# Optimization experiments

Measured on AMD Instinct MI355X. Metric: run time of the kernel, lower is better.

## Reference

```python
import jax, jax.numpy as jnp
import numpy as np

B, N, D = 8, 2048, 768
LN_EPS = 1e-5


def setup_inputs() -> dict:
    key = jax.random.key(0)
    ks = jax.random.split(key, 5)
    scale = 1.0 / np.sqrt(D)
    features = jax.random.normal(ks[0], (B, N, D), dtype=jnp.float32)
    mask = jax.random.randint(ks[1], (B, N), 0, 2) == 1  # True = masked (padding)
    Wq = jax.random.normal(ks[2], (D, D), dtype=jnp.float32) * scale
    Wk = jax.random.normal(ks[3], (D, D), dtype=jnp.float32) * scale
    Wv = jax.random.normal(ks[4], (D, D), dtype=jnp.float32) * scale
    ln_gamma = jnp.ones((D,), dtype=jnp.float32)
    ln_beta = jnp.zeros((D,), dtype=jnp.float32)
    return {"features": features, "mask": mask, "Wq": Wq, "Wk": Wk, "Wv": Wv,
            "ln_gamma": ln_gamma, "ln_beta": ln_beta}


def reference(features, mask, Wq, Wk, Wv, ln_gamma, ln_beta):
    # LayerNorm over last dim
    mu = jnp.mean(features, axis=-1, keepdims=True)
    var = jnp.mean(jnp.square(features - mu), axis=-1, keepdims=True)
    x = (features - mu) * jax.lax.rsqrt(var + LN_EPS) * ln_gamma + ln_beta
    # torch Linear: y = x @ W.T
    Q = jnp.einsum('bnd,ed->bne', x, Wq)
    K = jnp.einsum('bnd,ed->bne', x, Wk)
    V = jnp.einsum('bnd,ed->bne', x, Wv)
    scale = x.shape[-1] ** -0.5
    scores = jnp.einsum('bnd,bmd->bnm', Q, K) * scale  # [B,N,N]
    scores = jnp.where(mask[:, None, :], -jnp.inf, scores)
    probs = jax.nn.softmax(scores, axis=-1)
    ctx = jnp.einsum('bnm,bmd->bnd', probs, V)
    return ctx
```

## Files before the change

kernel.cpp:

```cpp
#include <hip/hip_runtime.h>
#include <hip/hip_bf16.h>
#include <cstdint>

typedef __attribute__((ext_vector_type(8))) __bf16 bf16v8;
typedef __attribute__((ext_vector_type(4))) float f32x4;
typedef __attribute__((ext_vector_type(4))) unsigned short ushort4v;
typedef __attribute__((ext_vector_type(8))) unsigned short ushort8v;

#define BB 8
#define NN 2048
#define DD 768

__device__ __forceinline__ float b2f(unsigned short u) {
  union { unsigned int i; float f; } c; c.i = ((unsigned int)u) << 16; return c.f;
}
__device__ __forceinline__ unsigned short f2b(float f) {
  union { float f; unsigned int i; } c; c.f = f;
  unsigned int u = c.i;
  return (unsigned short)((u + 0x7fffu + ((u >> 16) & 1u)) >> 16);
}

__global__ __launch_bounds__(256) void ln_kernel(const float* __restrict__ x,
                                                 const float* __restrict__ gamma,
                                                 const float* __restrict__ beta,
                                                 unsigned short* __restrict__ xb) {
  int row = blockIdx.x;
  const float* xr = x + (size_t)row * DD;
  int t = threadIdx.x;
  float a0 = xr[t], a1 = xr[t + 256], a2 = xr[t + 512];
  float s = a0 + a1 + a2;
  float q = a0 * a0 + a1 * a1 + a2 * a2;
  for (int o = 32; o > 0; o >>= 1) { s += __shfl_xor(s, o); q += __shfl_xor(q, o); }
  __shared__ float red[2][4];
  int w = t >> 6, lane = t & 63;
  if (lane == 0) { red[0][w] = s; red[1][w] = q; }
  __syncthreads();
  s = red[0][0] + red[0][1] + red[0][2] + red[0][3];
  q = red[1][0] + red[1][1] + red[1][2] + red[1][3];
  float mean = s * (1.0f / DD);
  float var = q * (1.0f / DD) - mean * mean;
  float inv = rsqrtf(var + 1e-5f);
  unsigned short* o0 = xb + (size_t)row * DD;
  o0[t]       = f2b((a0 - mean) * inv * gamma[t]       + beta[t]);
  o0[t + 256] = f2b((a1 - mean) * inv * gamma[t + 256] + beta[t + 256]);
  o0[t + 512] = f2b((a2 - mean) * inv * gamma[t + 512] + beta[t + 512]);
}

__global__ __launch_bounds__(256) void wconvert(const float* __restrict__ Wq,
                                                const float* __restrict__ Wk,
                                                const float* __restrict__ Wv,
                                                unsigned short* __restrict__ Wcat) {
  int i = blockIdx.x * 256 + threadIdx.x;
  const int dd = DD * DD;
  if (i >= 3 * dd) return;
  float v;
  if (i < dd)           v = Wq[i] * 0.03608439182435161f;
  else if (i < 2 * dd)  v = Wk[i - dd];
  else                  v = Wv[i - 2 * dd];
  Wcat[i] = f2b(v);
}

__global__ __launch_bounds__(256) void mask_scan(const int* __restrict__ mask,
                                                 int* __restrict__ kidx,
                                                 int* __restrict__ ncnt) {
  int b = blockIdx.x;
  const int* mr = mask + b * NN;
  int t = threadIdx.x;
#pragma unroll
  for (int j = 0; j < 8; ++j) kidx[b * NN + t * 8 + j] = 0;
  int v[8]; int s = 0;
#pragma unroll
  for (int j = 0; j < 8; ++j) { v[j] = (mr[t * 8 + j] == 0) ? 1 : 0; s += v[j]; }
  int lane = t & 63, w = t >> 6;
  int x = s;
  for (int o = 1; o < 64; o <<= 1) { int y = __shfl_up(x, o); if (lane >= o) x += y; }
  __shared__ int wsum[4];
  if (lane == 63) wsum[w] = x;
  __syncthreads();
  int base = 0;
#pragma unroll
  for (int i = 0; i < 4; ++i) if (i < w) base += wsum[i];
  int run = base + x - s;
#pragma unroll
  for (int j = 0; j < 8; ++j) { if (v[j]) kidx[b * NN + run] = t * 8 + j; run += v[j]; }
  if (t == 255) ncnt[b] = base + x;
}

__global__ __launch_bounds__(256) void vtc_gather(const unsigned short* __restrict__ Vt,
                                                  const int* __restrict__ kidx,
                                                  const int* __restrict__ ncnt,
                                                  unsigned short* __restrict__ Vtc) {
  int be = blockIdx.x;
  int b = be / DD;
  int nc = ncnt[b];
  int r128 = (nc + 127) & ~127;
  const unsigned short* src = Vt + (size_t)be * NN;
  unsigned short* dst = Vtc + (size_t)be * NN;
  const int* kx = kidx + b * NN;
  for (int c = threadIdx.x; c < r128; c += 256)
    dst[c] = (c < nc) ? src[kx[c]] : (unsigned short)0;
}

__device__ __forceinline__ void gload_lds16(const void* g, void* l) {
  __builtin_amdgcn_global_load_lds(
      (const __attribute__((address_space(1))) void*)g,
      (__attribute__((address_space(3))) void*)(unsigned)(uintptr_t)l,
      16, 0, 0);
}

#define RDA(i0, ks, B)                                                                   \
  _Pragma("unroll")                                                                      \
  for (int i_ = 0; i_ < 4; ++i_)                                                         \
    aq[i_] = *(const bf16v8*)&smem[(B) + (ks) * 8192 + arow0 + ((i0) + i_) * 512 + kg8];
#define RDB(ks, B)                                                                       \
  _Pragma("unroll")                                                                      \
  for (int j_ = 0; j_ < NJ; ++j_)                                                        \
    bq[j_] = *(const bf16v8*)&smem[(B) + 16384 + (ks) * 8192 + brow0 + j_ * 512 + kg8];
#define MFQ(i0)                                                                          \
  _Pragma("unroll")                                                                      \
  for (int i_ = 0; i_ < 4; ++i_) {                                                       \
    _Pragma("unroll")                                                                    \
    for (int j_ = 0; j_ < NJ; ++j_)                                                      \
      acc[(i0) + i_][j_] = __builtin_amdgcn_mfma_f32_16x16x32_bf16(                      \
          aq[i_], bq[j_], acc[(i0) + i_][j_], 0, 0, 0);                                  \
  }
#define BARF asm volatile("s_barrier" ::: "memory")
#define VMC6 asm volatile("s_waitcnt vmcnt(6)" ::: "memory")
#define VMC0 asm volatile("s_waitcnt vmcnt(0)" ::: "memory")
#define P1   __builtin_amdgcn_s_setprio(1)
#define P0   __builtin_amdgcn_s_setprio(0)

#define TILEK(KT, CURB, NXTB)                                                            \
  do {                                                                                   \
    RDA(0, 0, CURB); RDB(0, CURB);                                                       \
    if ((KT) + 1 < NT) stgA((KT) + 1, 1, (NXTB));                                        \
    BARF; P1; MFQ(0); P0; BARF;                                                          \
    RDA(4, 0, CURB);                                                                     \
    if ((KT) + 1 < NT) stgB((KT) + 1, 1, (NXTB));                                        \
    BARF; P1; MFQ(4); P0;                                                                \
    VMC6; BARF;                                                                          \
    RDA(0, 1, CURB); RDB(1, CURB);                                                       \
    if ((KT) + 2 < NT) stgA((KT) + 2, 0, (CURB));                                        \
    BARF; P1; MFQ(0); P0; BARF;                                                          \
    RDA(4, 1, CURB);                                                                     \
    if ((KT) + 2 < NT) stgB((KT) + 2, 0, (CURB));                                        \
    BARF; P1; MFQ(4); P0;                                                                \
    if ((KT) < NT - 2) { VMC6; } else { VMC0; }                                          \
    BARF;                                                                                \
  } while (0)

template <int MODE, int NJ>
__global__ __launch_bounds__(512, 2) void gemm256(
    const unsigned short* __restrict__ A, const unsigned short* __restrict__ Bm,
    unsigned short* __restrict__ Cq, unsigned short* __restrict__ Ck,
    unsigned short* __restrict__ Cv, float* __restrict__ Cf,
    int K, int lda, int ldb,
    long aStride, long bStride, long cStride,
    const int* __restrict__ ncnt) {
  extern __shared__ unsigned short smem[];
  const int BN = NJ * 64;

  const int t = threadIdx.x;
  int bx = blockIdx.x, by = blockIdx.y, bz = blockIdx.z;
  {
    const int gx = gridDim.x, gy = gridDim.y;
    const int nwg = gx * gy * (int)gridDim.z;
    int id = bx + gx * (by + gy * bz);
    int sw = (id & 7) * (nwg >> 3) + (id >> 3);
    bx = sw % gx; int r2 = sw / gx;
    by = r2 % gy; bz = r2 / gy;
  }
  const int n0 = bx * BN, m0 = by * 256;
  const int NT = (MODE == 2) ? (((ncnt[bz] + 127) >> 7) << 1) : (K >> 6);

  const unsigned short* Ab = A + (size_t)bz * aStride;
  const unsigned short* Bb = Bm + (size_t)bz * bStride;

  const int lane = t & 63;
  const int w = t >> 6;
  const int wm = w >> 2, wn = w & 3;
  const int frow = lane & 15;
  const int kg8 = (lane >> 4) * 8;
  const int arow0 = (wm * 128 + frow) * 32;
  const int brow0 = (wn * (NJ * 16) + frow) * 32;

  const int srow = t >> 2;
  const int scol8 = (t & 3) * 8;
  const unsigned short* Asrc = Ab + (size_t)(m0 + srow) * lda + scol8;
  const unsigned short* Bsrc = Bb + (size_t)(n0 + srow) * ldb + scol8;
  const int sdst = w * 512;

  auto stgA = [&](int kt, int ks, int bufb) {
    const unsigned short* s = Asrc + kt * 64 + ks * 32;
    gload_lds16(s, &smem[bufb + ks * 8192 + sdst]);
    gload_lds16(s + (size_t)128 * lda, &smem[bufb + ks * 8192 + 4096 + sdst]);
  };
  auto stgB = [&](int kt, int ks, int bufb) {
    const unsigned short* s = Bsrc + kt * 64 + ks * 32;
    gload_lds16(s, &smem[bufb + 16384 + ks * 8192 + sdst]);
    gload_lds16(s + (size_t)128 * ldb, &smem[bufb + 16384 + ks * 8192 + 4096 + sdst]);
  };

  f32x4 acc[8][NJ] = {};
  bf16v8 aq[4], bq[NJ];

  stgA(0, 0, 0);     stgB(0, 0, 0);
  stgA(0, 1, 0);     stgB(0, 1, 0);
  stgA(1, 0, 32768); stgB(1, 0, 32768);
  asm volatile("s_waitcnt vmcnt(8)" ::: "memory");
  BARF;

  for (int ktp = 0; ktp < NT; ktp += 2) {
    TILEK(ktp, 0, 32768);
    TILEK(ktp + 1, 32768, 0);
  }

  const int r0 = (lane >> 4) * 4;
  const int c0 = lane & 15;
  const int mrowB = m0 + wm * 128 + r0;
  const int ncolB = n0 + wn * (NJ * 16) + c0;

  if (MODE == 0) {
    if (n0 < 1536) {
      unsigned short* dst = (n0 < 768) ? Cq : Ck;
      const int cb = (n0 < 768) ? 0 : 768;
#pragma unroll
      for (int i = 0; i < 8; ++i)
#pragma unroll
        for (int j = 0; j < NJ; ++j)
#pragma unroll
          for (int r = 0; r < 4; ++r)
            dst[(size_t)(mrowB + i * 16 + r) * DD + (ncolB + j * 16 - cb)] = f2b(acc[i][j][r]);
    } else {
#pragma unroll
      for (int i = 0; i < 8; ++i) {
        int row = mrowB + i * 16;
        int bb = row >> 11, nn = row & 2047;
#pragma unroll
        for (int j = 0; j < NJ; ++j) {
          int e = ncolB + j * 16 - 1536;
          ushort4v pk;
#pragma unroll
          for (int r = 0; r < 4; ++r) pk[r] = f2b(acc[i][j][r]);
          *(ushort4v*)&Cv[((size_t)(bb * DD + e)) * NN + nn] = pk;
        }
      }
    }
  } else {
    float* dst = Cf + (size_t)bz * cStride;
#pragma unroll
    for (int i = 0; i < 8; ++i)
#pragma unroll
      for (int j = 0; j < NJ; ++j)
#pragma unroll
        for (int r = 0; r < 4; ++r)
          dst[(size_t)(mrowB + i * 16 + r) * DD + (ncolB + j * 16)] = acc[i][j][r];
  }
}

template <int NJ, int NTT>
__global__ __launch_bounds__(512, 2) void gemm1P(
    const unsigned short* __restrict__ Qa, const unsigned short* __restrict__ Kn,
    unsigned short* __restrict__ So, const int* __restrict__ kidx,
    const int* __restrict__ ncnt, int lda, int ldb) {
  extern __shared__ unsigned short smem[];
  constexpr int NT = NTT;

  const int t = threadIdx.x;
  const int lane = t & 63;
  const int w = t >> 6;
  const int wm = w >> 2, wn = w & 3;
  const int frow = lane & 15;
  const int kg8 = (lane >> 4) * 8;
  const int arow0 = (wm * 128 + frow) * 32;
  const int brow0 = (wn * (NJ * 16) + frow) * 32;
  const int srow = t >> 2;
  const int scol8 = (t & 3) * 8;
  const int sdst = w * 512;
  const int r0 = (lane >> 4) * 4;
  const int c0 = lane & 15;

  int nbv[8];
#pragma unroll
  for (int b_ = 0; b_ < 8; ++b_) nbv[b_] = (ncnt[b_] + 255) >> 8;

  f32x4 acc[8][NJ];
  bf16v8 aq[4], bq[NJ];

#pragma unroll 1
  for (int it = 0; it < 2; ++it) {
    int rem = (int)blockIdx.x + it * 256;
    int b = 0;
#pragma unroll 1
    for (; b < 8; ++b) { int c = nbv[b] * 8; if (rem < c) break; rem -= c; }
    if (b >= 8) break;
    const int ni = rem >> 3, mi = rem & 7;
    const int m0 = mi * 256, n0 = ni * 256;

    const unsigned short* Asrc = Qa + ((size_t)b * NN + m0 + srow) * lda + scol8;
    const int kv0 = kidx[b * NN + n0 + srow];
    const int kv1 = kidx[b * NN + n0 + 128 + srow];
    const unsigned short* Bsrc0 = Kn + ((size_t)b * NN + kv0) * ldb + scol8;
    const unsigned short* Bsrc1 = Kn + ((size_t)b * NN + kv1) * ldb + scol8;

    auto stgA = [&](int kt, int ks, int bufb) {
      const unsigned short* s = Asrc + kt * 64 + ks * 32;
      gload_lds16(s, &smem[bufb + ks * 8192 + sdst]);
      gload_lds16(s + (size_t)128 * lda, &smem[bufb + ks * 8192 + 4096 + sdst]);
    };
    auto stgB = [&](int kt, int ks, int bufb) {
      gload_lds16(Bsrc0 + kt * 64 + ks * 32, &smem[bufb + 16384 + ks * 8192 + sdst]);
      gload_lds16(Bsrc1 + kt * 64 + ks * 32, &smem[bufb + 16384 + ks * 8192 + 4096 + sdst]);
    };

#pragma unroll
    for (int i = 0; i < 8; ++i)
#pragma unroll
      for (int j = 0; j < NJ; ++j) acc[i][j] = f32x4{0.f, 0.f, 0.f, 0.f};

    stgA(0, 0, 0);     stgB(0, 0, 0);
    stgA(0, 1, 0);     stgB(0, 1, 0);
    stgA(1, 0, 32768); stgB(1, 0, 32768);
    asm volatile("s_waitcnt vmcnt(8)" ::: "memory");
    BARF;

    for (int ktp = 0; ktp < NT; ktp += 2) {
      TILEK(ktp, 0, 32768);
      TILEK(ktp + 1, 32768, 0);
    }

    unsigned short* dst = So + (size_t)b * NN * NN;
    const int mrowB = m0 + wm * 128 + r0;
    const int ncolB = n0 + wn * (NJ * 16) + c0;
#pragma unroll
    for (int i = 0; i < 8; ++i)
#pragma unroll
      for (int j = 0; j < NJ; ++j)
#pragma unroll
        for (int r = 0; r < 4; ++r)
          dst[(size_t)(mrowB + i * 16 + r) * NN + (ncolB + j * 16)] = f2b(acc[i][j][r]);
  }
}

__global__ __launch_bounds__(256) void softmax_c(unsigned short* __restrict__ S,
                                                 const int* __restrict__ ncnt) {
  int row = blockIdx.x;
  int bb = row >> 11;
  const int nc = ncnt[bb];
  const int p128 = (nc + 127) & ~127;
  unsigned short* sr = S + (size_t)row * NN;
  int t = threadIdx.x;
  const int cbase = t * 8;

  float v[8];
  const bool anyload = cbase < nc;
  ushort8v pk;
  if (anyload) pk = *(const ushort8v*)&sr[cbase];
  float mx = -1e30f;
#pragma unroll
  for (int j = 0; j < 8; ++j) {
    v[j] = anyload ? b2f(pk[j]) : 0.f;
    if (cbase + j < nc) mx = fmaxf(mx, v[j]);
  }
  for (int o = 32; o > 0; o >>= 1) mx = fmaxf(mx, __shfl_xor(mx, o));
  __shared__ float redm[4], reds[4];
  int w = t >> 6, lane = t & 63;
  if (lane == 0) redm[w] = mx;
  __syncthreads();
  mx = fmaxf(fmaxf(redm[0], redm[1]), fmaxf(redm[2], redm[3]));

  float e[8];
  float sum = 0.f;
#pragma unroll
  for (int j = 0; j < 8; ++j) {
    e[j] = (cbase + j < nc) ? __expf(v[j] - mx) : 0.f;
    sum += e[j];
  }
  for (int o = 32; o > 0; o >>= 1) sum += __shfl_xor(sum, o);
  if (lane == 0) reds[w] = sum;
  __syncthreads();
  sum = reds[0] + reds[1] + reds[2] + reds[3];
  float inv = 1.0f / sum;

  if (cbase < p128) {
    ushort8v op;
#pragma unroll
    for (int j = 0; j < 8; ++j) op[j] = f2b(e[j] * inv);
    *(ushort8v*)&sr[cbase] = op;
  }
}

extern "C" void kernel_launch(void* const* d_in, const int* in_sizes, int n_in,
                              void* d_out, int out_size, void* d_ws, size_t ws_size,
                              hipStream_t stream) {
  const float* features = (const float*)d_in[0];
  const int* mask       = (const int*)d_in[1];
  const float* Wq       = (const float*)d_in[2];
  const float* Wk       = (const float*)d_in[3];
  const float* Wv       = (const float*)d_in[4];
  const float* gamma    = (const float*)d_in[5];
  const float* beta     = (const float*)d_in[6];
  float* out = (float*)d_out;

  char* ws = (char*)d_ws;
  size_t off = 0;
  auto alloc = [&](size_t bytes) {
    char* p = ws + off;
    off += (bytes + 255) & ~(size_t)255;
    return p;
  };
  unsigned short* Wcat = (unsigned short*)alloc((size_t)(2304 + 64) * DD * 2);
  unsigned short* Qb   = (unsigned short*)alloc((size_t)BB * NN * DD * 2);
  unsigned short* Kb   = (unsigned short*)alloc((size_t)BB * NN * DD * 2);
  unsigned short* Vt   = (unsigned short*)alloc(((size_t)BB * DD + 64) * NN * 2);
  int* kidx = (int*)alloc((size_t)BB * NN * 4);
  int* ncnt = (int*)alloc(64 * 4);
  char* last = alloc((size_t)BB * NN * NN * 2);
  unsigned short* Sb = (unsigned short*)last;
  unsigned short* Xb = (unsigned short*)last;
  unsigned short* Vtc = Qb;

  (void)hipFuncSetAttribute(reinterpret_cast<const void*>(&gemm256<0, 3>),
                            hipFuncAttributeMaxDynamicSharedMemorySize, 131072);
  (void)hipFuncSetAttribute(reinterpret_cast<const void*>(&gemm1P<4, 12>),
                            hipFuncAttributeMaxDynamicSharedMemorySize, 131072);
  (void)hipFuncSetAttribute(reinterpret_cast<const void*>(&gemm256<2, 3>),
                            hipFuncAttributeMaxDynamicSharedMemorySize, 131072);

  ln_kernel<<<BB * NN, 256, 0, stream>>>(features, gamma, beta, Xb);
  wconvert<<<(3 * DD * DD + 255) / 256, 256, 0, stream>>>(Wq, Wk, Wv, Wcat);
  mask_scan<<<BB, 256, 0, stream>>>(mask, kidx, ncnt);

  gemm256<0, 3><<<dim3(2304 / 192, (BB * NN) / 256, 1), 512, 131072, stream>>>(
      Xb, Wcat, Qb, Kb, Vt, nullptr, DD, DD, DD, 0, 0, 0, ncnt);

  gemm1P<4, 12><<<256, 512, 131072, stream>>>(Qb, Kb, Sb, kidx, ncnt, DD, DD);

  vtc_gather<<<BB * DD, 256, 0, stream>>>(Vt, kidx, ncnt, Vtc);

  softmax_c<<<BB * NN, 256, 0, stream>>>(Sb, ncnt);

  gemm256<2, 3><<<dim3(DD / 192, NN / 256, BB), 512, 131072, stream>>>(
      Sb, Vtc, nullptr, nullptr, nullptr, out, NN, NN, NN,
      (long)NN * NN, (long)DD * NN, (long)NN * DD, ncnt);
}
```

Measured before the change: 225.1 us.

## Compute K and V projections only for unmasked keys via compacted inputs

Unmasked rows of the normalized input are gathered into a compacted buffer first. A dedicated K/V projection GEMM then runs only over those rows and writes compacted K and transposed V directly, while the Q projection stays a separate full GEMM. This drops the index-gathered B loads in the score GEMM and the separate V gather kernel, and skips projecting masked keys (about half of them). It adds a new gather kernel and per-batch offset bookkeeping, and splits the one fused QKV launch into two.

```diff
diff --git a/kernel.cpp b/kernel.cpp
--- a/kernel.cpp
+++ b/kernel.cpp
@@ -86,19 +86,31 @@
   if (t == 255) ncnt[b] = base + x;
 }
 
-__global__ __launch_bounds__(256) void vtc_gather(const unsigned short* __restrict__ Vt,
-                                                  const int* __restrict__ kidx,
-                                                  const int* __restrict__ ncnt,
-                                                  unsigned short* __restrict__ Vtc) {
-  int be = blockIdx.x;
-  int b = be / DD;
-  int nc = ncnt[b];
-  int r128 = (nc + 127) & ~127;
-  const unsigned short* src = Vt + (size_t)be * NN;
-  unsigned short* dst = Vtc + (size_t)be * NN;
-  const int* kx = kidx + b * NN;
-  for (int c = threadIdx.x; c < r128; c += 256)
-    dst[c] = (c < nc) ? src[kx[c]] : (unsigned short)0;
+__global__ __launch_bounds__(256) void xc_gather(const unsigned short* __restrict__ Xb,
+                                                 const int* __restrict__ kidx,
+                                                 const int* __restrict__ ncnt,
+                                                 unsigned short* __restrict__ Xc) {
+  const int b = blockIdx.y;
+  const int nc = ncnt[b];
+  const int r256 = (nc + 255) & ~255;
+  const int row0 = blockIdx.x * 32;
+  if (row0 >= r256) return;
+  int off = 0;
+#pragma unroll
+  for (int i = 0; i < 8; ++i) if (i < b) off += (ncnt[i] + 255) & ~255;
+  const int t = threadIdx.x;
+  for (int r = 0; r < 32; ++r) {
+    const int rl = row0 + r;
+    unsigned short* dst = Xc + (size_t)(off + rl) * DD;
+    if (t < 96) {
+      if (rl < nc) {
+        const unsigned short* src = Xb + ((size_t)b * NN + kidx[b * NN + rl]) * DD;
+        *(ushort8v*)&dst[t * 8] = *(const ushort8v*)&src[t * 8];
+      } else {
+        *(ushort8v*)&dst[t * 8] = ushort8v{0, 0, 0, 0, 0, 0, 0, 0};
+      }
+    }
+  }
 }
 
 __device__ __forceinline__ void gload_lds16(const void* g, void* l) {
@@ -152,8 +164,7 @@
 template <int MODE, int NJ>
 __global__ __launch_bounds__(512, 2) void gemm256(
     const unsigned short* __restrict__ A, const unsigned short* __restrict__ Bm,
-    unsigned short* __restrict__ Cq, unsigned short* __restrict__ Ck,
-    unsigned short* __restrict__ Cv, float* __restrict__ Cf,
+    unsigned short* __restrict__ Cq, float* __restrict__ Cf,
     int K, int lda, int ldb,
     long aStride, long bStride, long cStride,
     const int* __restrict__ ncnt) {
@@ -220,49 +231,120 @@
   const int mrowB = m0 + wm * 128 + r0;
   const int ncolB = n0 + wn * (NJ * 16) + c0;
 
-  if (MODE == 0) {
-    if (n0 < 1536) {
-      unsigned short* dst = (n0 < 768) ? Cq : Ck;
-      const int cb = (n0 < 768) ? 0 : 768;
-#pragma unroll
-      for (int i = 0; i < 8; ++i)
-#pragma unroll
-        for (int j = 0; j < NJ; ++j)
-#pragma unroll
-          for (int r = 0; r < 4; ++r)
-            dst[(size_t)(mrowB + i * 16 + r) * DD + (ncolB + j * 16 - cb)] = f2b(acc[i][j][r]);
-    } else {
-#pragma unroll
-      for (int i = 0; i < 8; ++i) {
-        int row = mrowB + i * 16;
-        int bb = row >> 11, nn = row & 2047;
-#pragma unroll
-        for (int j = 0; j < NJ; ++j) {
-          int e = ncolB + j * 16 - 1536;
-          ushort4v pk;
-#pragma unroll
-          for (int r = 0; r < 4; ++r) pk[r] = f2b(acc[i][j][r]);
-          *(ushort4v*)&Cv[((size_t)(bb * DD + e)) * NN + nn] = pk;
-        }
+  if (MODE == 3) {
+#pragma unroll
+    for (int i = 0; i < 8; ++i)
+#pragma unroll
+      for (int j = 0; j < NJ; ++j)
+#pragma unroll
+        for (int r = 0; r < 4; ++r)
+          Cq[(size_t)(mrowB + i * 16 + r) * DD + (ncolB + j * 16)] = f2b(acc[i][j][r]);
+  } else {
+    float* dst = Cf + (size_t)bz * cStride;
+#pragma unroll
+    for (int i = 0; i < 8; ++i)
+#pragma unroll
+      for (int j = 0; j < NJ; ++j)
+#pragma unroll
+        for (int r = 0; r < 4; ++r)
+          dst[(size_t)(mrowB + i * 16 + r) * DD + (ncolB + j * 16)] = acc[i][j][r];
+  }
+}
+
+template <int NJ, int NTT>
+__global__ __launch_bounds__(512, 2) void gemmKV(
+    const unsigned short* __restrict__ Xc, const unsigned short* __restrict__ Wcat,
+    unsigned short* __restrict__ Kc, unsigned short* __restrict__ Vtc,
+    const int* __restrict__ ncnt) {
+  extern __shared__ unsigned short smem[];
+  constexpr int NT = NTT;
+
+  int offv[9]; offv[0] = 0;
+#pragma unroll
+  for (int i = 0; i < 8; ++i) offv[i + 1] = offv[i] + ((ncnt[i] + 255) & ~255);
+  const int GT = offv[8] >> 8;
+  const int id = (int)blockIdx.x;
+  if (id >= GT * 8) return;
+  const int gt = id >> 3, ni = id & 7;
+  int b = 0;
+#pragma unroll
+  for (int i = 1; i < 8; ++i) if (offv[i] <= gt * 256) b = i;
+  const int off_b = offv[b];
+
+  const int t = threadIdx.x;
+  const int lane = t & 63;
+  const int w = t >> 6;
+  const int wm = w >> 2, wn = w & 3;
+  const int frow = lane & 15;
+  const int kg8 = (lane >> 4) * 8;
+  const int arow0 = (wm * 128 + frow) * 32;
+  const int brow0 = (wn * (NJ * 16) + frow) * 32;
+  const int srow = t >> 2;
+  const int scol8 = (t & 3) * 8;
+  const int sdst = w * 512;
+
+  const unsigned short* Asrc = Xc + (size_t)(gt * 256 + srow) * DD + scol8;
+  const unsigned short* Bsrc = Wcat + (size_t)(768 + ni * (NJ * 64) + srow) * DD + scol8;
+
+  auto stgA = [&](int kt, int ks, int bufb) {
+    const unsigned short* s = Asrc + kt * 64 + ks * 32;
+    gload_lds16(s, &smem[bufb + ks * 8192 + sdst]);
+    gload_lds16(s + (size_t)128 * DD, &smem[bufb + ks * 8192 + 4096 + sdst]);
+  };
+  auto stgB = [&](int kt, int ks, int bufb) {
+    const unsigned short* s = Bsrc + kt * 64 + ks * 32;
+    gload_lds16(s, &smem[bufb + 16384 + ks * 8192 + sdst]);
+    gload_lds16(s + (size_t)128 * DD, &smem[bufb + 16384 + ks * 8192 + 4096 + sdst]);
+  };
+
+  f32x4 acc[8][NJ] = {};
+  bf16v8 aq[4], bq[NJ];
+
+  stgA(0, 0, 0);     stgB(0, 0, 0);
+  stgA(0, 1, 0);     stgB(0, 1, 0);
+  stgA(1, 0, 32768); stgB(1, 0, 32768);
+  asm volatile("s_waitcnt vmcnt(8)" ::: "memory");
+  BARF;
+
+  for (int ktp = 0; ktp < NT; ktp += 2) {
+    TILEK(ktp, 0, 32768);
+    TILEK(ktp + 1, 32768, 0);
+  }
+
+  const int r0 = (lane >> 4) * 4;
+  const int c0 = lane & 15;
+  const int rowL = wm * 128 + r0;
+  const int ncolL = ni * (NJ * 64) + wn * (NJ * 16) + c0;
+  const int cbase = gt * 256 - off_b + rowL;
+
+  if (ni < 4) {
+    unsigned short* dst = Kc + (size_t)b * NN * DD;
+#pragma unroll
+    for (int i = 0; i < 8; ++i)
+#pragma unroll
+      for (int j = 0; j < NJ; ++j)
+#pragma unroll
+        for (int r = 0; r < 4; ++r)
+          dst[(size_t)(cbase + i * 16 + r) * DD + (ncolL + j * 16)] = f2b(acc[i][j][r]);
+  } else {
+#pragma unroll
+    for (int i = 0; i < 8; ++i) {
+#pragma unroll
+      for (int j = 0; j < NJ; ++j) {
+        const int e = ncolL + j * 16 - 768;
+        ushort4v pk;
+#pragma unroll
+        for (int r = 0; r < 4; ++r) pk[r] = f2b(acc[i][j][r]);
+        *(ushort4v*)&Vtc[((size_t)b * DD + e) * NN + cbase + i * 16] = pk;
       }
     }
-  } else {
-    float* dst = Cf + (size_t)bz * cStride;
-#pragma unroll
-    for (int i = 0; i < 8; ++i)
-#pragma unroll
-      for (int j = 0; j < NJ; ++j)
-#pragma unroll
-        for (int r = 0; r < 4; ++r)
-          dst[(size_t)(mrowB + i * 16 + r) * DD + (ncolB + j * 16)] = acc[i][j][r];
   }
 }
 
 template <int NJ, int NTT>
 __global__ __launch_bounds__(512, 2) void gemm1P(
     const unsigned short* __restrict__ Qa, const unsigned short* __restrict__ Kn,
-    unsigned short* __restrict__ So, const int* __restrict__ kidx,
-    const int* __restrict__ ncnt, int lda, int ldb) {
+    unsigned short* __restrict__ So, const int* __restrict__ ncnt, int lda, int ldb) {
   extern __shared__ unsigned short smem[];
   constexpr int NT = NTT;
 
@@ -298,10 +380,7 @@
     const int m0 = mi * 256, n0 = ni * 256;
 
     const unsigned short* Asrc = Qa + ((size_t)b * NN + m0 + srow) * lda + scol8;
-    const int kv0 = kidx[b * NN + n0 + srow];
-    const int kv1 = kidx[b * NN + n0 + 128 + srow];
-    const unsigned short* Bsrc0 = Kn + ((size_t)b * NN + kv0) * ldb + scol8;
-    const unsigned short* Bsrc1 = Kn + ((size_t)b * NN + kv1) * ldb + scol8;
+    const unsigned short* Bsrc = Kn + ((size_t)b * NN + n0 + srow) * ldb + scol8;
 
     auto stgA = [&](int kt, int ks, int bufb) {
       const unsigned short* s = Asrc + kt * 64 + ks * 32;
@@ -309,8 +388,9 @@
       gload_lds16(s + (size_t)128 * lda, &smem[bufb + ks * 8192 + 4096 + sdst]);
     };
     auto stgB = [&](int kt, int ks, int bufb) {
-      gload_lds16(Bsrc0 + kt * 64 + ks * 32, &smem[bufb + 16384 + ks * 8192 + sdst]);
-      gload_lds16(Bsrc1 + kt * 64 + ks * 32, &smem[bufb + 16384 + ks * 8192 + 4096 + sdst]);
+      const unsigned short* s = Bsrc + kt * 64 + ks * 32;
+      gload_lds16(s, &smem[bufb + 16384 + ks * 8192 + sdst]);
+      gload_lds16(s + (size_t)128 * ldb, &smem[bufb + 16384 + ks * 8192 + 4096 + sdst]);
     };
 
 #pragma unroll
@@ -411,16 +491,18 @@
   };
   unsigned short* Wcat = (unsigned short*)alloc((size_t)(2304 + 64) * DD * 2);
   unsigned short* Qb   = (unsigned short*)alloc((size_t)BB * NN * DD * 2);
-  unsigned short* Kb   = (unsigned short*)alloc((size_t)BB * NN * DD * 2);
-  unsigned short* Vt   = (unsigned short*)alloc(((size_t)BB * DD + 64) * NN * 2);
+  unsigned short* Kc   = (unsigned short*)alloc((size_t)BB * NN * DD * 2);
+  unsigned short* Vtc  = (unsigned short*)alloc(((size_t)BB * DD + 64) * NN * 2);
   int* kidx = (int*)alloc((size_t)BB * NN * 4);
   int* ncnt = (int*)alloc(64 * 4);
   char* last = alloc((size_t)BB * NN * NN * 2);
   unsigned short* Sb = (unsigned short*)last;
   unsigned short* Xb = (unsigned short*)last;
-  unsigned short* Vtc = Qb;
-
-  (void)hipFuncSetAttribute(reinterpret_cast<const void*>(&gemm256<0, 3>),
+  unsigned short* Xc = (unsigned short*)(last + (size_t)34 * 1024 * 1024);
+
+  (void)hipFuncSetAttribute(reinterpret_cast<const void*>(&gemm256<3, 3>),
+                            hipFuncAttributeMaxDynamicSharedMemorySize, 131072);
+  (void)hipFuncSetAttribute(reinterpret_cast<const void*>(&gemmKV<3, 12>),
                             hipFuncAttributeMaxDynamicSharedMemorySize, 131072);
   (void)hipFuncSetAttribute(reinterpret_cast<const void*>(&gemm1P<4, 12>),
                             hipFuncAttributeMaxDynamicSharedMemorySize, 131072);
@@ -430,17 +512,18 @@
   ln_kernel<<<BB * NN, 256, 0, stream>>>(features, gamma, beta, Xb);
   wconvert<<<(3 * DD * DD + 255) / 256, 256, 0, stream>>>(Wq, Wk, Wv, Wcat);
   mask_scan<<<BB, 256, 0, stream>>>(mask, kidx, ncnt);
-
-  gemm256<0, 3><<<dim3(2304 / 192, (BB * NN) / 256, 1), 512, 131072, stream>>>(
-      Xb, Wcat, Qb, Kb, Vt, nullptr, DD, DD, DD, 0, 0, 0, ncnt);
-
-  gemm1P<4, 12><<<256, 512, 131072, stream>>>(Qb, Kb, Sb, kidx, ncnt, DD, DD);
-
-  vtc_gather<<<BB * DD, 256, 0, stream>>>(Vt, kidx, ncnt, Vtc);
+  xc_gather<<<dim3(64, BB), 256, 0, stream>>>(Xb, kidx, ncnt, Xc);
+
+  gemm256<3, 3><<<dim3(4, 64, 1), 512, 131072, stream>>>(
+      Xb, Wcat, Qb, nullptr, DD, DD, DD, 0, 0, 0, ncnt);
+
+  gemmKV<3, 12><<<512, 512, 131072, stream>>>(Xc, Wcat, Kc, Vtc, ncnt);
+
+  gemm1P<4, 12><<<256, 512, 131072, stream>>>(Qb, Kc, Sb, ncnt, DD, DD);
 
   softmax_c<<<BB * NN, 256, 0, stream>>>(Sb, ncnt);
 
   gemm256<2, 3><<<dim3(DD / 192, NN / 256, BB), 512, 131072, stream>>>(
-      Sb, Vtc, nullptr, nullptr, nullptr, out, NN, NN, NN,
+      Sb, Vtc, nullptr, out, NN, NN, NN,
       (long)NN * NN, (long)DD * NN, (long)NN * DD, ncnt);
 }
```

Result: no change. 223.5 us (-0.7%).
